# Kernel tuning notes

Measured on AMD Instinct MI355X. Metric: run time of the kernel, lower is better.

Reference implementation:

```python
import jax, jax.numpy as jnp
import numpy as np

B, S, D, H = 8, 1024, 1024, 16
DK = D // H


def setup_inputs() -> dict:
    key = jax.random.key(0)
    ks = jax.random.split(key, 12)
    sc = 1.0 / np.sqrt(D)
    return {
        "query": jax.random.normal(ks[0], (B, S, D), jnp.float32),
        "key": jax.random.normal(ks[1], (B, S, D), jnp.float32),
        "value": jax.random.normal(ks[2], (B, S, D), jnp.float32),
        "Wq": jax.random.normal(ks[3], (D, D), jnp.float32) * sc,
        "bq": jnp.zeros((D,), jnp.float32),
        "Wk": jax.random.normal(ks[4], (D, D), jnp.float32) * sc,
        "bk": jnp.zeros((D,), jnp.float32),
        "Wv": jax.random.normal(ks[5], (D, D), jnp.float32) * sc,
        "bv": jnp.zeros((D,), jnp.float32),
        "Wa": jax.random.normal(ks[6], (D, D), jnp.float32) * sc,
        "ba": jnp.zeros((D,), jnp.float32),
        "qvec": jax.random.normal(ks[7], (D,), jnp.float32),
    }


def reference(query, key, value, Wq, bq, Wk, bk, Wv, bv, Wa, ba, qvec):
    # project and split heads: [B,S,D] -> [B,H,S,DK]
    def split(x, W, b):
        y = x @ W.T + b
        return y.reshape(B, S, H, DK).transpose(0, 2, 1, 3)

    q = split(query, Wq, bq)
    k = split(key, Wk, bk)
    v = split(value, Wv, bv)

    scores = jnp.einsum('bhqd,bhkd->bhqk', q, k) / jnp.sqrt(jnp.float32(DK))
    p = jax.nn.softmax(scores, axis=-1)          # dropout p=0 -> identity
    x = jnp.einsum('bhqk,bhkd->bhqd', p, v)
    x = x.transpose(0, 2, 1, 3).reshape(B, S, D)  # [B,S,D]

    # attention2 pooling head
    a = jnp.tanh(x @ Wa.T + ba) @ qvec           # [B,S]
    alpha = jax.nn.softmax(a, axis=-1)
    return jnp.einsum('bs,bsd->bd', alpha, x)    # [B,D]
```

## Files before the change

kernel.cpp:

```cpp
#include <hip/hip_runtime.h>

typedef __bf16 bf16;
typedef __attribute__((ext_vector_type(8))) __bf16 bf16x8;
typedef __attribute__((ext_vector_type(4))) __bf16 bf16x4;
typedef __attribute__((ext_vector_type(4))) float f32x4;

#define GLDS16(g, l) __builtin_amdgcn_global_load_lds( \
    (const __attribute__((address_space(1))) void*)(g), \
    (__attribute__((address_space(3))) void*)(l), 16, 0, 0)

#define MFMA16(a, b, c) __builtin_amdgcn_mfma_f32_16x16x32_bf16(a, b, c, 0, 0, 0)

#define TR16(dst, addr, off) \
  asm volatile("ds_read_b64_tr_b16 %0, %1 offset:" #off : "=v"(dst) : "v"(addr))

struct CvtArgs { const float* in[4]; bf16* out[4]; };

__global__ __launch_bounds__(256) void f2b_multi(CvtArgs a, int n8) {
  int i = blockIdx.x * 256 + threadIdx.x;
  if (i >= n8) return;
  const float* in = a.in[blockIdx.y];
  bf16* out = a.out[blockIdx.y];
  const f32x4* p = (const f32x4*)in + (size_t)i * 2;
  f32x4 x = p[0], y = p[1];
  bf16x8 o;
  o[0] = (bf16)x[0]; o[1] = (bf16)x[1]; o[2] = (bf16)x[2]; o[3] = (bf16)x[3];
  o[4] = (bf16)y[0]; o[5] = (bf16)y[1]; o[6] = (bf16)y[2]; o[7] = (bf16)y[3];
  ((bf16x8*)out)[i] = o;
}

template <int EPI>
__device__ __forceinline__ void gemm_body(
    const bf16* __restrict__ A, const bf16* __restrict__ Bw,
    const float* __restrict__ bias, const float* __restrict__ qv,
    bf16* __restrict__ C, float* __restrict__ aout, const int N, const int K) {
  __shared__ __attribute__((aligned(16))) bf16 As[8192];
  __shared__ __attribute__((aligned(16))) bf16 Bs[8192];
  const int tid = threadIdx.x;
  const int wid = tid >> 6, lane = tid & 63;
  const int g = lane >> 4, lc = lane & 15;
  const int row0 = blockIdx.x * 128, col0 = blockIdx.y * 128;
  const int wr = wid >> 1, wc = wid & 1;

  const int c0 = tid, c1 = tid + 256;
  const bf16* gA0 = A + ((size_t)(row0 + (c0 & 127)) * K + (c0 >> 7) * 8);
  const bf16* gA1 = A + ((size_t)(row0 + (c1 & 127)) * K + (c1 >> 7) * 8);
  const bf16* gB0 = Bw + ((size_t)(col0 + (c0 & 127)) * K + (c0 >> 7) * 8);
  const bf16* gB1 = Bw + ((size_t)(col0 + (c1 & 127)) * K + (c1 >> 7) * 8);
  bf16* lA0 = As + (size_t)(wid * 64) * 8;
  bf16* lA1 = As + (size_t)(256 + wid * 64) * 8;
  bf16* lB0 = Bs + (size_t)(wid * 64) * 8;
  bf16* lB1 = Bs + (size_t)(256 + wid * 64) * 8;

  const f32x4 z4 = {0.f, 0.f, 0.f, 0.f};
  f32x4 acc[4][4];
#pragma unroll
  for (int m = 0; m < 4; ++m)
#pragma unroll
    for (int n = 0; n < 4; ++n) acc[m][n] = z4;

  GLDS16(gA0, lA0);
  GLDS16(gA1, lA1);
  GLDS16(gB0, lB0);
  GLDS16(gB1, lB1);

  for (int kt = 0; kt < K; kt += 32) {
    __syncthreads();
    const int cur = (kt >> 5) & 1;
    if (kt + 32 < K) {
      const int nb = cur ^ 1;
      GLDS16(gA0 + kt + 32, lA0 + nb * 4096);
      GLDS16(gA1 + kt + 32, lA1 + nb * 4096);
      GLDS16(gB0 + kt + 32, lB0 + nb * 4096);
      GLDS16(gB1 + kt + 32, lB1 + nb * 4096);
    }
    const bf16* Ab = As + cur * 4096;
    const bf16* Bb = Bs + cur * 4096;
    bf16x8 af[4], bfv[4];
#pragma unroll
    for (int m = 0; m < 4; ++m)
      af[m] = *(const bf16x8*)(Ab + g * 1024 + (wr * 64 + m * 16 + lc) * 8);
#pragma unroll
    for (int n = 0; n < 4; ++n)
      bfv[n] = *(const bf16x8*)(Bb + g * 1024 + (wc * 64 + n * 16 + lc) * 8);
#pragma unroll
    for (int m = 0; m < 4; ++m)
#pragma unroll
      for (int n = 0; n < 4; ++n)
        acc[m][n] = MFMA16(af[m], bfv[n], acc[m][n]);
  }

  if constexpr (EPI == 0) {
#pragma unroll
    for (int n = 0; n < 4; ++n) {
      const int col = col0 + wc * 64 + n * 16 + lc;
      const float bb = bias[col];
#pragma unroll
      for (int m = 0; m < 4; ++m)
#pragma unroll
        for (int r = 0; r < 4; ++r) {
          const int row = row0 + wr * 64 + m * 16 + g * 4 + r;
          C[(size_t)row * N + col] = (bf16)(acc[m][n][r] + bb);
        }
    }
  } else {
    float part[4][4];
#pragma unroll
    for (int m = 0; m < 4; ++m)
#pragma unroll
      for (int r = 0; r < 4; ++r) part[m][r] = 0.f;
#pragma unroll
    for (int n = 0; n < 4; ++n) {
      const int col = col0 + wc * 64 + n * 16 + lc;
      const float bb = bias[col];
      const float qq = qv[col];
#pragma unroll
      for (int m = 0; m < 4; ++m)
#pragma unroll
        for (int r = 0; r < 4; ++r)
          part[m][r] += tanhf(acc[m][n][r] + bb) * qq;
    }
#pragma unroll
    for (int m = 0; m < 4; ++m)
#pragma unroll
      for (int r = 0; r < 4; ++r) {
        float v = part[m][r];
        v += __shfl_xor(v, 1); v += __shfl_xor(v, 2);
        v += __shfl_xor(v, 4); v += __shfl_xor(v, 8);
        if (lc == 0) {
          const int row = row0 + wr * 64 + m * 16 + g * 4 + r;
          atomicAdd(&aout[row], v);
        }
      }
  }
}

struct GemmSet { const bf16* A; const bf16* Bw; const float* bias; bf16* C; };
struct Gemm3Args { GemmSet s[3]; };

__global__ __launch_bounds__(256) void gemm3_kernel(Gemm3Args a) {
  const GemmSet s = a.s[blockIdx.z];
  gemm_body<0>(s.A, s.Bw, s.bias, nullptr, s.C, nullptr, 1024, 1024);
}

__global__ __launch_bounds__(256) void gemm_a_kernel(
    const bf16* __restrict__ A, const bf16* __restrict__ Bw,
    const float* __restrict__ bias, const float* __restrict__ qv,
    float* __restrict__ aout) {
  gemm_body<1>(A, Bw, bias, qv, nullptr, aout, 1024, 1024);
}

__global__ __launch_bounds__(256) void attn_kernel(
    const bf16* __restrict__ qp, const bf16* __restrict__ kp,
    const bf16* __restrict__ vp, bf16* __restrict__ xb, float* __restrict__ xf) {
  constexpr int S = 1024, D = 1024;
  __shared__ __attribute__((aligned(16))) bf16 Ks[8192];
  __shared__ __attribute__((aligned(16))) bf16 Vs[8192];
  __shared__ __attribute__((aligned(16))) bf16 Ps[4096];
  const int tid = threadIdx.x, wid = tid >> 6, lane = tid & 63;
  const int g = lane >> 4, lc = lane & 15;
  const int b = blockIdx.x >> 4, h = blockIdx.x & 15;
  const int q0 = blockIdx.y * 64;
  const size_t base = (size_t)b * S * D + (size_t)h * 64;

  bf16x8 qf[2];
  {
    const bf16* qrow = qp + base + (size_t)(q0 + wid * 16 + lc) * D;
    qf[0] = *(const bf16x8*)(qrow + g * 8);
    qf[1] = *(const bf16x8*)(qrow + 32 + g * 8);
#pragma unroll
    for (int j = 0; j < 8; ++j) {
      qf[0][j] = (bf16)((float)qf[0][j] * 0.125f);
      qf[1][j] = (bf16)((float)qf[1][j] * 0.125f);
    }
  }
  float m_s = -1e30f, l_s = 0.f;
  const f32x4 z4 = {0.f, 0.f, 0.f, 0.f};
  f32x4 ax[4];
#pragma unroll
  for (int m = 0; m < 4; ++m) ax[m] = z4;

  const int c0 = tid, c1 = tid + 256;
  const bf16* gK0 = kp + base + (size_t)(c0 & 63) * D + (c0 >> 6) * 8;
  const bf16* gK1 = kp + base + (size_t)(c1 & 63) * D + (c1 >> 6) * 8;
  bf16* lK0 = Ks + (size_t)(c0 - lane) * 8;
  bf16* lK1 = Ks + (size_t)(c1 - lane) * 8;
  const bf16* gV0 = vp + base + (size_t)((c0 >> 5) * 4 + ((c0 >> 1) & 3)) * D +
                    ((c0 >> 3) & 3) * 16 + (c0 & 1) * 8;
  const bf16* gV1 = vp + base + (size_t)((c1 >> 5) * 4 + ((c1 >> 1) & 3)) * D +
                    ((c1 >> 3) & 3) * 16 + (c1 & 1) * 8;
  bf16* lV0 = Vs + (size_t)(c0 - lane) * 8;
  bf16* lV1 = Vs + (size_t)(c1 - lane) * 8;

  bf16* pw = Ps + wid * 1024;
  const int pswz_a = lc & 3, pswz_b = (lc >> 2) & 3;
  const unsigned vaddr0 =
      (unsigned)(uintptr_t)(const __attribute__((address_space(3))) bf16*)(Vs + 512 * g + 4 * lc);

  GLDS16(gK0, lK0);
  GLDS16(gK1, lK1);
  GLDS16(gV0, lV0);
  GLDS16(gV1, lV1);

  for (int t = 0; t < 16; ++t) {
    __syncthreads();
    const int cur = t & 1;
    if (t < 15) {
      const size_t off = (size_t)(t + 1) * 64 * D;
      const int nb = cur ^ 1;
      GLDS16(gK0 + off, lK0 + nb * 4096);
      GLDS16(gK1 + off, lK1 + nb * 4096);
      GLDS16(gV0 + off, lV0 + nb * 4096);
      GLDS16(gV1 + off, lV1 + nb * 4096);
    }
    const bf16* Kb = Ks + cur * 4096;
    const unsigned va = vaddr0 + cur * 8192u;

    f32x4 sc[4];
    __builtin_amdgcn_s_setprio(1);
#pragma unroll
    for (int m = 0; m < 4; ++m) {
      f32x4 z = z4;
      bf16x8 kf0 = *(const bf16x8*)(Kb + (size_t)g * 512 + (m * 16 + lc) * 8);
      bf16x8 kf1 = *(const bf16x8*)(Kb + (size_t)(4 + g) * 512 + (m * 16 + lc) * 8);
      z = MFMA16(kf0, qf[0], z);
      z = MFMA16(kf1, qf[1], z);
      sc[m] = z;
    }
    __builtin_amdgcn_s_setprio(0);

    float mx = -1e30f;
#pragma unroll
    for (int m = 0; m < 4; ++m)
      mx = fmaxf(mx, fmaxf(fmaxf(sc[m][0], sc[m][1]), fmaxf(sc[m][2], sc[m][3])));
    mx = fmaxf(mx, __shfl_xor(mx, 16));
    mx = fmaxf(mx, __shfl_xor(mx, 32));
    if (!__all(mx - m_s <= 8.f)) {
      const float mn = fmaxf(m_s, mx);
      const float cr = __expf(m_s - mn);
      l_s *= cr;
#pragma unroll
      for (int m = 0; m < 4; ++m) ax[m] *= cr;
      m_s = mn;
    }
    float sm = 0.f;
#pragma unroll
    for (int m = 0; m < 4; ++m)
#pragma unroll
      for (int r = 0; r < 4; ++r) {
        float p = __expf(sc[m][r] - m_s);
        sc[m][r] = p;
        sm += p;
      }
    sm += __shfl_xor(sm, 16);
    sm += __shfl_xor(sm, 32);
    l_s += sm;

#pragma unroll
    for (int m = 0; m < 4; ++m) {
      bf16x4 pk;
      pk[0] = (bf16)sc[m][0]; pk[1] = (bf16)sc[m][1];
      pk[2] = (bf16)sc[m][2]; pk[3] = (bf16)sc[m][3];
      *(bf16x4*)(pw + lc * 64 + 16 * (m ^ pswz_a) + 4 * (g ^ pswz_b)) = pk;
    }

    bf16x4 pr[2][2];
#pragma unroll
    for (int kk = 0; kk < 2; ++kk)
#pragma unroll
      for (int jh = 0; jh < 2; ++jh) {
        const int msrc = 2 * kk + (g >> 1);
        const int gsrc = (2 * g + jh) & 3;
        pr[kk][jh] = *(const bf16x4*)(pw + lc * 64 + 16 * (msrc ^ pswz_a) + 4 * (gsrc ^ pswz_b));
      }
    bf16x8 pf0 = __builtin_shufflevector(pr[0][0], pr[0][1], 0, 1, 2, 3, 4, 5, 6, 7);
    bf16x8 pf1 = __builtin_shufflevector(pr[1][0], pr[1][1], 0, 1, 2, 3, 4, 5, 6, 7);

    bf16x4 vt[4][2][2];
    TR16(vt[0][0][0], va, 0);    TR16(vt[1][0][0], va, 128);
    TR16(vt[2][0][0], va, 256);  TR16(vt[3][0][0], va, 384);
    TR16(vt[0][0][1], va, 512);  TR16(vt[1][0][1], va, 640);
    TR16(vt[2][0][1], va, 768);  TR16(vt[3][0][1], va, 896);
    TR16(vt[0][1][0], va, 4096); TR16(vt[1][1][0], va, 4224);
    TR16(vt[2][1][0], va, 4352); TR16(vt[3][1][0], va, 4480);
    TR16(vt[0][1][1], va, 4608); TR16(vt[1][1][1], va, 4736);
    TR16(vt[2][1][1], va, 4864); TR16(vt[3][1][1], va, 4992);
    asm volatile("s_waitcnt lgkmcnt(0)" ::: "memory");
    __builtin_amdgcn_sched_barrier(0);

    __builtin_amdgcn_s_setprio(1);
#pragma unroll
    for (int md = 0; md < 4; ++md) {
      bf16x8 a0 = __builtin_shufflevector(vt[md][0][0], vt[md][0][1], 0, 1, 2, 3, 4, 5, 6, 7);
      bf16x8 a1 = __builtin_shufflevector(vt[md][1][0], vt[md][1][1], 0, 1, 2, 3, 4, 5, 6, 7);
      ax[md] = MFMA16(a0, pf0, ax[md]);
      ax[md] = MFMA16(a1, pf1, ax[md]);
    }
    __builtin_amdgcn_s_setprio(0);
  }

  const float inv = 1.0f / l_s;
  const int qrow = q0 + wid * 16 + lc;
  float* xfr = xf + base + (size_t)qrow * D;
  bf16* xbr = xb + base + (size_t)qrow * D;
#pragma unroll
  for (int m = 0; m < 4; ++m) {
    f32x4 vv = ax[m] * inv;
    *(f32x4*)(xfr + 16 * m + 4 * g) = vv;
    bf16x4 bb;
    bb[0] = (bf16)vv[0]; bb[1] = (bf16)vv[1];
    bb[2] = (bf16)vv[2]; bb[3] = (bf16)vv[3];
    *(bf16x4*)(xbr + 16 * m + 4 * g) = bb;
  }
}

__global__ __launch_bounds__(256) void softmax_rows(const float* __restrict__ av,
                                                    float* __restrict__ alpha) {
  const int b = blockIdx.x, t = threadIdx.x;
  __shared__ float red[8];
  f32x4 v = *(const f32x4*)(av + b * 1024 + t * 4);
  float m = fmaxf(fmaxf(v[0], v[1]), fmaxf(v[2], v[3]));
#pragma unroll
  for (int o = 1; o < 64; o <<= 1) m = fmaxf(m, __shfl_xor(m, o));
  if ((t & 63) == 0) red[t >> 6] = m;
  __syncthreads();
  m = fmaxf(fmaxf(red[0], red[1]), fmaxf(red[2], red[3]));
  f32x4 e;
  float s = 0.f;
#pragma unroll
  for (int j = 0; j < 4; ++j) { e[j] = __expf(v[j] - m); s += e[j]; }
#pragma unroll
  for (int o = 1; o < 64; o <<= 1) s += __shfl_xor(s, o);
  if ((t & 63) == 0) red[4 + (t >> 6)] = s;
  __syncthreads();
  const float inv = 1.0f / (red[4] + red[5] + red[6] + red[7]);
  *(f32x4*)(alpha + b * 1024 + t * 4) = e * inv;
}

__global__ __launch_bounds__(256) void pool_kernel(const float* __restrict__ xf,
                                                   const float* __restrict__ alpha,
                                                   float* __restrict__ out) {
  const int b = blockIdx.y, sc = blockIdx.x, t = threadIdx.x;
  f32x4 acc = {0.f, 0.f, 0.f, 0.f};
  const float* xrow = xf + (size_t)b * 1024 * 1024;
  for (int s = sc * 64; s < sc * 64 + 64; ++s) {
    const float al = alpha[b * 1024 + s];
    f32x4 xv = *(const f32x4*)(xrow + (size_t)s * 1024 + t * 4);
    acc += xv * al;
  }
  atomicAdd(&out[b * 1024 + t * 4 + 0], acc[0]);
  atomicAdd(&out[b * 1024 + t * 4 + 1], acc[1]);
  atomicAdd(&out[b * 1024 + t * 4 + 2], acc[2]);
  atomicAdd(&out[b * 1024 + t * 4 + 3], acc[3]);
}

extern "C" void kernel_launch(void* const* d_in, const int* in_sizes, int n_in,
                              void* d_out, int out_size, void* d_ws, size_t ws_size,
                              hipStream_t stream) {
  const float* Q   = (const float*)d_in[0];
  const float* K   = (const float*)d_in[1];
  const float* V   = (const float*)d_in[2];
  const float* Wq  = (const float*)d_in[3];
  const float* bq  = (const float*)d_in[4];
  const float* Wk  = (const float*)d_in[5];
  const float* bk  = (const float*)d_in[6];
  const float* Wv  = (const float*)d_in[7];
  const float* bv  = (const float*)d_in[8];
  const float* Wa  = (const float*)d_in[9];
  const float* ba  = (const float*)d_in[10];
  const float* qvec = (const float*)d_in[11];
  float* out = (float*)d_out;
  char* ws = (char*)d_ws;
  const size_t MB = 1ull << 20;

  bf16* Wqb = (bf16*)(ws + 0 * MB);
  bf16* Wkb = (bf16*)(ws + 2 * MB);
  bf16* Wvb = (bf16*)(ws + 4 * MB);
  bf16* Wab = (bf16*)(ws + 6 * MB);
  bf16* qb  = (bf16*)(ws + 8 * MB);
  bf16* kb  = (bf16*)(ws + 24 * MB);
  bf16* vb  = (bf16*)(ws + 40 * MB);
  bf16* qp  = (bf16*)(ws + 56 * MB);
  bf16* kp  = (bf16*)(ws + 72 * MB);
  bf16* vp  = (bf16*)(ws + 88 * MB);
  float* av    = (float*)(ws + 104 * MB);
  float* alpha = (float*)(ws + 104 * MB + 65536);
  bf16* xb  = qb;
  float* xf = (float*)(ws + 24 * MB);

  hipMemsetAsync(av, 0, 8192 * sizeof(float), stream);
  hipMemsetAsync(out, 0, 8192 * sizeof(float), stream);

  CvtArgs cq = {{Q, K, V, nullptr}, {qb, kb, vb, nullptr}};
  f2b_multi<<<dim3(4096, 3), 256, 0, stream>>>(cq, 1048576);
  CvtArgs cw = {{Wq, Wk, Wv, Wa}, {Wqb, Wkb, Wvb, Wab}};
  f2b_multi<<<dim3(512, 4), 256, 0, stream>>>(cw, 131072);

  Gemm3Args g3 = {{{qb, Wqb, bq, qp}, {kb, Wkb, bk, kp}, {vb, Wvb, bv, vp}}};
  gemm3_kernel<<<dim3(64, 8, 3), 256, 0, stream>>>(g3);

  attn_kernel<<<dim3(128, 16), 256, 0, stream>>>(qp, kp, vp, xb, xf);

  gemm_a_kernel<<<dim3(64, 8), 256, 0, stream>>>(xb, Wab, ba, qvec, av);

  softmax_rows<<<8, 256, 0, stream>>>(av, alpha);
  pool_kernel<<<dim3(16, 8), 256, 0, stream>>>(xf, alpha, out);
}
```

Measured before the change: 266.9 us.

## Fuse fp32-to-bf16 input conversion into the QKV projection GEMM

Removes the separate conversion pass over the query, key and value activations. The projection GEMM now loads fp32 A tiles into registers, converts them to bf16 and stores them to LDS itself. This saves a full write and reread of 48MB of bf16 intermediates. In exchange, the GEMM drops LDS double buffering and now uses a single buffer with two barriers per k-step, which exposes load latency. It also reads fp32 data, so A traffic doubles, and the same single-buffer change applies to the attention-output GEMM.

```diff
diff --git a/kernel.cpp b/kernel.cpp
--- a/kernel.cpp
+++ b/kernel.cpp
@@ -29,13 +29,14 @@
   ((bf16x8*)out)[i] = o;
 }
 
-template <int EPI>
+template <int EPI, int CVT>
 __device__ __forceinline__ void gemm_body(
-    const bf16* __restrict__ A, const bf16* __restrict__ Bw,
-    const float* __restrict__ bias, const float* __restrict__ qv,
-    bf16* __restrict__ C, float* __restrict__ aout, const int N, const int K) {
-  __shared__ __attribute__((aligned(16))) bf16 As[8192];
-  __shared__ __attribute__((aligned(16))) bf16 Bs[8192];
+    const float* __restrict__ Af, const bf16* __restrict__ Ab,
+    const bf16* __restrict__ Bw, const float* __restrict__ bias,
+    const float* __restrict__ qv, bf16* __restrict__ C,
+    float* __restrict__ aout, const int N, const int K) {
+  __shared__ __attribute__((aligned(16))) bf16 As[4096];
+  __shared__ __attribute__((aligned(16))) bf16 Bs[4096];
   const int tid = threadIdx.x;
   const int wid = tid >> 6, lane = tid & 63;
   const int g = lane >> 4, lc = lane & 15;
@@ -43,14 +44,22 @@
   const int wr = wid >> 1, wc = wid & 1;
 
   const int c0 = tid, c1 = tid + 256;
-  const bf16* gA0 = A + ((size_t)(row0 + (c0 & 127)) * K + (c0 >> 7) * 8);
-  const bf16* gA1 = A + ((size_t)(row0 + (c1 & 127)) * K + (c1 >> 7) * 8);
   const bf16* gB0 = Bw + ((size_t)(col0 + (c0 & 127)) * K + (c0 >> 7) * 8);
   const bf16* gB1 = Bw + ((size_t)(col0 + (c1 & 127)) * K + (c1 >> 7) * 8);
-  bf16* lA0 = As + (size_t)(wid * 64) * 8;
-  bf16* lA1 = As + (size_t)(256 + wid * 64) * 8;
-  bf16* lB0 = Bs + (size_t)(wid * 64) * 8;
-  bf16* lB1 = Bs + (size_t)(256 + wid * 64) * 8;
+  bf16* lB0 = Bs + (size_t)(c0 - lane) * 8;
+  bf16* lB1 = Bs + (size_t)(c1 - lane) * 8;
+  const float* fA0 = nullptr; const float* fA1 = nullptr;
+  const bf16* gA0 = nullptr; const bf16* gA1 = nullptr;
+  bf16* lA0 = nullptr; bf16* lA1 = nullptr;
+  if constexpr (CVT) {
+    fA0 = Af + ((size_t)(row0 + (c0 & 127)) * K + (c0 >> 7) * 8);
+    fA1 = Af + ((size_t)(row0 + (c1 & 127)) * K + (c1 >> 7) * 8);
+  } else {
+    gA0 = Ab + ((size_t)(row0 + (c0 & 127)) * K + (c0 >> 7) * 8);
+    gA1 = Ab + ((size_t)(row0 + (c1 & 127)) * K + (c1 >> 7) * 8);
+    lA0 = As + (size_t)(c0 - lane) * 8;
+    lA1 = As + (size_t)(c1 - lane) * 8;
+  }
 
   const f32x4 z4 = {0.f, 0.f, 0.f, 0.f};
   f32x4 acc[4][4];
@@ -59,30 +68,51 @@
 #pragma unroll
     for (int n = 0; n < 4; ++n) acc[m][n] = z4;
 
-  GLDS16(gA0, lA0);
-  GLDS16(gA1, lA1);
-  GLDS16(gB0, lB0);
-  GLDS16(gB1, lB1);
+  f32x4 ar0, ar1, ar2, ar3;
+  if constexpr (CVT) {
+    ar0 = *(const f32x4*)(fA0);
+    ar1 = *(const f32x4*)(fA0 + 4);
+    ar2 = *(const f32x4*)(fA1);
+    ar3 = *(const f32x4*)(fA1 + 4);
+  }
 
   for (int kt = 0; kt < K; kt += 32) {
-    __syncthreads();
-    const int cur = (kt >> 5) & 1;
-    if (kt + 32 < K) {
-      const int nb = cur ^ 1;
-      GLDS16(gA0 + kt + 32, lA0 + nb * 4096);
-      GLDS16(gA1 + kt + 32, lA1 + nb * 4096);
-      GLDS16(gB0 + kt + 32, lB0 + nb * 4096);
-      GLDS16(gB1 + kt + 32, lB1 + nb * 4096);
-    }
-    const bf16* Ab = As + cur * 4096;
-    const bf16* Bb = Bs + cur * 4096;
+    if constexpr (CVT) {
+      bf16x8 w0, w1;
+#pragma unroll
+      for (int j = 0; j < 4; ++j) {
+        w0[j] = (bf16)ar0[j]; w0[4 + j] = (bf16)ar1[j];
+        w1[j] = (bf16)ar2[j]; w1[4 + j] = (bf16)ar3[j];
+      }
+      __syncthreads();
+      *(bf16x8*)(As + (size_t)c0 * 8) = w0;
+      *(bf16x8*)(As + (size_t)c1 * 8) = w1;
+      GLDS16(gB0 + kt, lB0);
+      GLDS16(gB1 + kt, lB1);
+      asm volatile("s_waitcnt vmcnt(0) lgkmcnt(0)" ::: "memory");
+      if (kt + 32 < K) {
+        ar0 = *(const f32x4*)(fA0 + kt + 32);
+        ar1 = *(const f32x4*)(fA0 + kt + 36);
+        ar2 = *(const f32x4*)(fA1 + kt + 32);
+        ar3 = *(const f32x4*)(fA1 + kt + 36);
+      }
+      __builtin_amdgcn_s_barrier();
+    } else {
+      __syncthreads();
+      GLDS16(gA0 + kt, lA0);
+      GLDS16(gA1 + kt, lA1);
+      GLDS16(gB0 + kt, lB0);
+      GLDS16(gB1 + kt, lB1);
+      __syncthreads();
+    }
+
     bf16x8 af[4], bfv[4];
 #pragma unroll
     for (int m = 0; m < 4; ++m)
-      af[m] = *(const bf16x8*)(Ab + g * 1024 + (wr * 64 + m * 16 + lc) * 8);
+      af[m] = *(const bf16x8*)(As + g * 1024 + (wr * 64 + m * 16 + lc) * 8);
 #pragma unroll
     for (int n = 0; n < 4; ++n)
-      bfv[n] = *(const bf16x8*)(Bb + g * 1024 + (wc * 64 + n * 16 + lc) * 8);
+      bfv[n] = *(const bf16x8*)(Bs + g * 1024 + (wc * 64 + n * 16 + lc) * 8);
 #pragma unroll
     for (int m = 0; m < 4; ++m)
 #pragma unroll
@@ -135,19 +165,19 @@
   }
 }
 
-struct GemmSet { const bf16* A; const bf16* Bw; const float* bias; bf16* C; };
+struct GemmSet { const float* Af; const bf16* Bw; const float* bias; bf16* C; };
 struct Gemm3Args { GemmSet s[3]; };
 
 __global__ __launch_bounds__(256) void gemm3_kernel(Gemm3Args a) {
   const GemmSet s = a.s[blockIdx.z];
-  gemm_body<0>(s.A, s.Bw, s.bias, nullptr, s.C, nullptr, 1024, 1024);
+  gemm_body<0, 1>(s.Af, nullptr, s.Bw, s.bias, nullptr, s.C, nullptr, 1024, 1024);
 }
 
 __global__ __launch_bounds__(256) void gemm_a_kernel(
     const bf16* __restrict__ A, const bf16* __restrict__ Bw,
     const float* __restrict__ bias, const float* __restrict__ qv,
     float* __restrict__ aout) {
-  gemm_body<1>(A, Bw, bias, qv, nullptr, aout, 1024, 1024);
+  gemm_body<1, 0>(nullptr, A, Bw, bias, qv, nullptr, aout, 1024, 1024);
 }
 
 __global__ __launch_bounds__(256) void attn_kernel(
@@ -377,26 +407,21 @@
   bf16* Wkb = (bf16*)(ws + 2 * MB);
   bf16* Wvb = (bf16*)(ws + 4 * MB);
   bf16* Wab = (bf16*)(ws + 6 * MB);
-  bf16* qb  = (bf16*)(ws + 8 * MB);
-  bf16* kb  = (bf16*)(ws + 24 * MB);
-  bf16* vb  = (bf16*)(ws + 40 * MB);
+  bf16* xb  = (bf16*)(ws + 8 * MB);
+  float* xf = (float*)(ws + 24 * MB);
   bf16* qp  = (bf16*)(ws + 56 * MB);
   bf16* kp  = (bf16*)(ws + 72 * MB);
   bf16* vp  = (bf16*)(ws + 88 * MB);
   float* av    = (float*)(ws + 104 * MB);
   float* alpha = (float*)(ws + 104 * MB + 65536);
-  bf16* xb  = qb;
-  float* xf = (float*)(ws + 24 * MB);
 
   hipMemsetAsync(av, 0, 8192 * sizeof(float), stream);
   hipMemsetAsync(out, 0, 8192 * sizeof(float), stream);
 
-  CvtArgs cq = {{Q, K, V, nullptr}, {qb, kb, vb, nullptr}};
-  f2b_multi<<<dim3(4096, 3), 256, 0, stream>>>(cq, 1048576);
   CvtArgs cw = {{Wq, Wk, Wv, Wa}, {Wqb, Wkb, Wvb, Wab}};
   f2b_multi<<<dim3(512, 4), 256, 0, stream>>>(cw, 131072);
 
-  Gemm3Args g3 = {{{qb, Wqb, bq, qp}, {kb, Wkb, bk, kp}, {vb, Wvb, bv, vp}}};
+  Gemm3Args g3 = {{{Q, Wqb, bq, qp}, {K, Wkb, bk, kp}, {V, Wvb, bv, vp}}};
   gemm3_kernel<<<dim3(64, 8, 3), 256, 0, stream>>>(g3);
 
   attn_kernel<<<dim3(128, 16), 256, 0, stream>>>(qp, kp, vp, xb, xf);
```

New measurement: 284.2 us. +6.5%, slower.
